# Kernel tuning notes

Measured on AMD Instinct MI355X. Metric: run time of the kernel, lower is better.

Reference implementation:

```python
import jax, jax.numpy as jnp
import numpy as np

D = 128  # h_dim == in_dim

def _gat_layer(h, d, src, dst, n_dst, W, U, V, a):
    # h: [N_src, Din], d: [E, 1], src/dst: [E]
    z = h @ W.T          # [N_src, D]
    zi = h @ U.T         # [N_src, D]
    t = d @ V.T          # [E, 1]
    Dh = W.shape[0]
    # attn_fc on concat([z_src, z_dst, t]) split into three partial dots
    e = z[src] @ a[:Dh] + z[dst] @ a[Dh:2 * Dh] + t[:, 0] * a[2 * Dh]
    e = jax.nn.leaky_relu(e)  # [E]
    # segment softmax over incoming edges of each dst node
    m = jax.ops.segment_max(e, dst, num_segments=n_dst)
    ex = jnp.exp(e - m[dst])
    s = jax.ops.segment_sum(ex, dst, num_segments=n_dst)
    alpha = ex / s[dst]  # [E]
    zn = jax.ops.segment_sum(alpha[:, None] * z[src], dst, num_segments=n_dst)
    return jax.nn.relu(zi[:n_dst] + zn)


def setup_inputs() -> dict:
    key = jax.random.key(0)
    ks = jax.random.split(key, 16)
    N0, ND0, ND1 = 100000, 40000, 20000
    E0, E1 = 640000, 320000
    sc = 1.0 / np.sqrt(D)
    inp = {
        "attr": jax.random.normal(ks[0], (N0, D), jnp.float32),
        "d0": jax.random.normal(ks[1], (E0, 1), jnp.float32),
        "d1": jax.random.normal(ks[2], (E1, 1), jnp.float32),
        "src0": jax.random.randint(ks[3], (E0,), 0, N0, jnp.int32),
        "dst0": jax.random.randint(ks[4], (E0,), 0, ND0, jnp.int32),
        "src1": jax.random.randint(ks[5], (E1,), 0, ND0, jnp.int32),
        "dst1": jax.random.randint(ks[6], (E1,), 0, ND1, jnp.int32),
        "n_dst0": ND0,
        "n_dst1": ND1,
        "W0": jax.random.normal(ks[7], (D, D), jnp.float32) * sc,
        "U0": jax.random.normal(ks[8], (D, D), jnp.float32) * sc,
        "V0": jax.random.normal(ks[9], (1, 1), jnp.float32),
        "a0": jax.random.normal(ks[10], (2 * D + 1,), jnp.float32) * sc,
        "W1": jax.random.normal(ks[11], (D, D), jnp.float32) * sc,
        "U1": jax.random.normal(ks[12], (D, D), jnp.float32) * sc,
        "V1": jax.random.normal(ks[13], (1, 1), jnp.float32),
        "a1": jax.random.normal(ks[14], (2 * D + 1,), jnp.float32) * sc,
    }
    return inp


def reference(attr, d0, d1, W0, U0, V0, a0, W1, U1, V1, a1,
              src0, dst0, src1, dst1, n_dst0, n_dst1):
    h = _gat_layer(attr, d0, src0, dst0, n_dst0, W0, U0, V0, a0)
    h = _gat_layer(h, d1, src1, dst1, n_dst1, W1, U1, V1, a1)
    return h
```

## Files before the change

kernel.cpp:

```cpp
#include <hip/hip_runtime.h>
#include <math.h>


#define D 128

typedef __bf16 bf16x8 __attribute__((ext_vector_type(8)));
typedef float f32x4 __attribute__((ext_vector_type(4)));

static __device__ __forceinline__ float lrelu(float x) {
  return x >= 0.f ? x : 0.01f * x;
}
static __device__ __forceinline__ unsigned short f2bf(float v) {
  unsigned int u = __float_as_uint(v);
  u += 0x7fffu + ((u >> 16) & 1u);
  return (unsigned short)(u >> 16);
}
static __device__ __forceinline__ float bf2f(unsigned short b) {
  return __uint_as_float((unsigned int)b << 16);
}

static __device__ __forceinline__ float4 loadV4(const float* p) {
  return *(const float4*)p;
}
static __device__ __forceinline__ float4 loadV4(const unsigned short* p) {
  ushort4 t = *(const ushort4*)p;
  return make_float4(bf2f(t.x), bf2f(t.y), bf2f(t.z), bf2f(t.w));
}
static __device__ __forceinline__ void storeV4(float* p, float4 v) {
  *(float4*)p = v;
}
static __device__ __forceinline__ void storeV4(unsigned short* p, float4 v) {
  ushort4 t;
  t.x = f2bf(v.x);
  t.y = f2bf(v.y);
  t.z = f2bf(v.z);
  t.w = f2bf(v.w);
  *(ushort4*)p = t;
}
static __device__ __forceinline__ void storeZi(float* p, float v) { *p = v; }
static __device__ __forceinline__ void storeZi(unsigned short* p, float v) {
  *p = f2bf(v);
}

static __device__ __forceinline__ int swz(int row, int colb) {
  return row * 256 + (colb ^ ((row & 7) << 4));
}

static __device__ __forceinline__ void count4(const int* __restrict__ dstC,
                                              int* __restrict__ cntC,
                                              int* __restrict__ rankC,
                                              int gid, int qC) {
  if (gid >= qC) return;
  int i0 = gid * 4;
  int4 d4 = *(const int4*)(dstC + i0);
  int4 r4;
  r4.x = atomicAdd(&cntC[d4.x], 1);
  r4.y = atomicAdd(&cntC[d4.y], 1);
  r4.z = atomicAdd(&cntC[d4.z], 1);
  r4.w = atomicAdd(&cntC[d4.w], 1);
  *(int4*)(rankC + i0) = r4;
}

__global__ __launch_bounds__(256) void cvt4_kernel(
    const float* __restrict__ s0, const float* __restrict__ s1,
    const float* __restrict__ s2, const float* __restrict__ s3,
    __bf16* __restrict__ dst) {
  int idx = blockIdx.x * 256 + threadIdx.x;
  const float* s = (idx < 16384) ? s0
                   : (idx < 32768) ? s1
                   : (idx < 49152) ? s2 : s3;
  dst[idx] = (__bf16)s[idx & 16383];
}

__global__ void zero_int_kernel(int* __restrict__ p, int n) {
  int i = blockIdx.x * 256 + threadIdx.x;
  if (i < n) p[i] = 0;
}

static __device__ __forceinline__ void stageA(const float* A, int rblk,
                                              int rlim, int t,
                                              unsigned char* ldsA) {
  const char* base = (const char*)A + (size_t)rblk * 512;
#pragma unroll
  for (int g = 0; g < 8; ++g) {
    int sb = g * 4096 + t * 16;
    float4 v = make_float4(0.f, 0.f, 0.f, 0.f);
    if (rblk + (sb >> 9) < rlim) v = *(const float4*)(base + sb);
    int db = sb >> 1;
    int row = db >> 8, colb = db & 255;
    ushort4 o;
    o.x = f2bf(v.x);
    o.y = f2bf(v.y);
    o.z = f2bf(v.z);
    o.w = f2bf(v.w);
    *(ushort4*)(&ldsA[swz(row, colb)]) = o;
  }
}
static __device__ __forceinline__ void stageA(const unsigned short* A,
                                              int rblk, int rlim, int t,
                                              unsigned char* ldsA) {
  const char* base = (const char*)A + (size_t)rblk * 256;
#pragma unroll
  for (int g = 0; g < 4; ++g) {
    int bi = g * 4096 + t * 16;
    int row = bi >> 8, colb = bi & 255;
    ushort4 lo = {0, 0, 0, 0}, hi = {0, 0, 0, 0};
    if (rblk + row < rlim) {
      lo = *(const ushort4*)(base + bi);
      hi = *(const ushort4*)(base + bi + 8);
    }
    *(ushort4*)(&ldsA[swz(row, colb)]) = lo;
    *(ushort4*)(&ldsA[swz(row, colb) + 8]) = hi;
  }
}

template <typename AT, typename ZiT>
__global__ __launch_bounds__(256, 3) void gemm_count(
    const AT* __restrict__ A, const __bf16* __restrict__ Wb,
    const __bf16* __restrict__ Ub, unsigned short* __restrict__ z,
    ZiT* __restrict__ zi, const float* __restrict__ a,
    float* __restrict__ zs, float* __restrict__ zd, int n_wb, int rows,
    int ndst, const int* __restrict__ dstC, int* __restrict__ cntC,
    int* __restrict__ rankC, int qC, int IL, int nC) {
  __shared__ unsigned char lds[49152];
  const int blk = blockIdx.x;
  const int t = threadIdx.x;

  if ((blk % IL) == 0 && (blk / IL) < nC) {
    count4(dstC, cntC, rankC, (blk / IL) * 256 + t, qC);
    return;
  }
  const int cb = min(nC, (blk + IL - 1) / IL);
  const int gb = blk - cb;

  const bool isU = (gb >= n_wb);
  const int rblk = (isU ? gb - n_wb : gb) * 64;
  const int rlim = isU ? ndst : rows;
  const __bf16* B = isU ? Ub : Wb;

#pragma unroll
  for (int g = 0; g < 8; ++g) {
    int bi = g * 4096 + t * 16;
    int row = bi >> 8, colb = bi & 255;
    bf16x8 v = *(const bf16x8*)((const char*)B + bi);
    *(bf16x8*)(&lds[swz(row, colb)]) = v;
  }
  stageA(A, rblk, rlim, t, lds + 32768);
  __syncthreads();

  const int wave = t >> 6;
  const int lane = t & 63;
  const int lm = lane & 15;
  const int lk = lane >> 4;
  const int r0 = rblk + wave * 16;
  if (r0 >= rlim) return;

  bf16x8 af[4];
#pragma unroll
  for (int kt = 0; kt < 4; ++kt) {
    int row = wave * 16 + lm;
    af[kt] = *(const bf16x8*)(&lds[32768 + swz(row, kt * 64 + lk * 16)]);
  }

  f32x4 acc[8];
#pragma unroll
  for (int tt = 0; tt < 8; ++tt) acc[tt] = (f32x4){0.f, 0.f, 0.f, 0.f};
#pragma unroll
  for (int kt = 0; kt < 4; ++kt) {
#pragma unroll
    for (int tt = 0; tt < 8; ++tt) {
      int row = tt * 16 + lm;
      bf16x8 bf = *(const bf16x8*)(&lds[swz(row, kt * 64 + lk * 16)]);
      acc[tt] =
          __builtin_amdgcn_mfma_f32_16x16x32_bf16(af[kt], bf, acc[tt], 0, 0, 0);
    }
  }

  if (!isU) {
#pragma unroll
    for (int tt = 0; tt < 8; ++tt)
#pragma unroll
      for (int rr = 0; rr < 4; ++rr)
        z[(size_t)(r0 + lk * 4 + rr) * D + tt * 16 + lm] = f2bf(acc[tt][rr]);

    float p1[4] = {0.f, 0.f, 0.f, 0.f};
    float p2[4] = {0.f, 0.f, 0.f, 0.f};
#pragma unroll
    for (int tt = 0; tt < 8; ++tt) {
      float a1 = a[tt * 16 + lm];
      float a2 = a[D + tt * 16 + lm];
#pragma unroll
      for (int rr = 0; rr < 4; ++rr) {
        p1[rr] += acc[tt][rr] * a1;
        p2[rr] += acc[tt][rr] * a2;
      }
    }
#pragma unroll
    for (int rr = 0; rr < 4; ++rr) {
#pragma unroll
      for (int o = 1; o < 16; o <<= 1) {
        p1[rr] += __shfl_xor(p1[rr], o);
        p2[rr] += __shfl_xor(p2[rr], o);
      }
      if (lm == 0) {
        zs[r0 + lk * 4 + rr] = p1[rr];
        zd[r0 + lk * 4 + rr] = p2[rr];
      }
    }
  } else {
#pragma unroll
    for (int tt = 0; tt < 8; ++tt)
#pragma unroll
      for (int rr = 0; rr < 4; ++rr)
        storeZi(&zi[(size_t)(r0 + lk * 4 + rr) * D + tt * 16 + lm],
                acc[tt][rr]);
  }
}

__global__ __launch_bounds__(256) void scan_partial(const int* __restrict__ cnt,
                                                    int* __restrict__ part,
                                                    int n) {
  __shared__ int sm[4];
  int base = blockIdx.x * 1024;
  int t = threadIdx.x;
  int s = 0;
#pragma unroll
  for (int i = 0; i < 4; ++i) {
    int idx = base + t + i * 256;
    s += (idx < n) ? cnt[idx] : 0;
  }
  for (int o = 32; o; o >>= 1) s += __shfl_xor(s, o);
  if ((t & 63) == 0) sm[t >> 6] = s;
  __syncthreads();
  if (t == 0) part[blockIdx.x] = sm[0] + sm[1] + sm[2] + sm[3];
}

__global__ __launch_bounds__(256) void scan_final(
    const int* __restrict__ cnt, const int* __restrict__ part,
    int* __restrict__ offs, int nb, int n, int total) {
  __shared__ int sm[4];
  __shared__ int sbase;
  int base = blockIdx.x * 1024;
  int t = threadIdx.x;
  if (t < 64) {
    int v = (t < nb && t < (int)blockIdx.x) ? part[t] : 0;
#pragma unroll
    for (int o = 32; o; o >>= 1) v += __shfl_xor(v, o);
    if (t == 0) sbase = v;
  }
  int idx = base + t * 4;
  int c0 = (idx + 0 < n) ? cnt[idx + 0] : 0;
  int c1 = (idx + 1 < n) ? cnt[idx + 1] : 0;
  int c2 = (idx + 2 < n) ? cnt[idx + 2] : 0;
  int c3 = (idx + 3 < n) ? cnt[idx + 3] : 0;
  int ts = c0 + c1 + c2 + c3;
  int v = ts;
#pragma unroll
  for (int o = 1; o < 64; o <<= 1) {
    int u = __shfl_up(v, o);
    if ((t & 63) >= o) v += u;
  }
  if ((t & 63) == 63) sm[t >> 6] = v;
  __syncthreads();
  int w = t >> 6;
  int waveoff = 0;
  if (w > 0) waveoff += sm[0];
  if (w > 1) waveoff += sm[1];
  if (w > 2) waveoff += sm[2];
  int run = v - ts + waveoff + sbase;
  if (idx + 0 < n) { offs[idx + 0] = run; run += c0; }
  if (idx + 1 < n) { offs[idx + 1] = run; run += c1; }
  if (idx + 2 < n) { offs[idx + 2] = run; run += c2; }
  if (idx + 3 < n) { offs[idx + 3] = run; run += c3; }
  if (blockIdx.x == 0 && t == 0) offs[n] = total;
}

__global__ void scatter_count(const int* __restrict__ src,
                              const int* __restrict__ dst,
                              const float* __restrict__ dE,
                              const float* __restrict__ zs,
                              const float* __restrict__ zd,
                              const float* __restrict__ V,
                              const float* __restrict__ a,
                              const int* __restrict__ rank,
                              const int* __restrict__ offs,
                              int2* __restrict__ csr, int E,
                              const int* __restrict__ dstC,
                              int* __restrict__ cntC, int* __restrict__ rankC,
                              int qC, int IL, int nC) {
  const int blk = blockIdx.x;
  const int t = threadIdx.x;
  if ((blk % IL) == 0 && (blk / IL) < nC) {
    count4(dstC, cntC, rankC, (blk / IL) * 256 + t, qC);
    return;
  }
  const int cb = min(nC, (blk + IL - 1) / IL);
  const int sb = blk - cb;

  int i0 = (sb * 256 + t) * 4;
  float vc = V[0] * a[2 * D];
  if (i0 + 4 <= E) {
    int4 s4 = *(const int4*)(src + i0);
    int4 d4 = *(const int4*)(dst + i0);
    float4 de = *(const float4*)(dE + i0);
    int4 r4 = *(const int4*)(rank + i0);
    float zs0 = zs[s4.x], zs1 = zs[s4.y], zs2 = zs[s4.z], zs3 = zs[s4.w];
    float zd0 = zd[d4.x], zd1 = zd[d4.y], zd2 = zd[d4.z], zd3 = zd[d4.w];
    int p0 = offs[d4.x] + r4.x;
    int p1 = offs[d4.y] + r4.y;
    int p2 = offs[d4.z] + r4.z;
    int p3 = offs[d4.w] + r4.w;
    float w0 = __expf(lrelu(zs0 + zd0 + de.x * vc));
    float w1 = __expf(lrelu(zs1 + zd1 + de.y * vc));
    float w2 = __expf(lrelu(zs2 + zd2 + de.z * vc));
    float w3 = __expf(lrelu(zs3 + zd3 + de.w * vc));
    csr[p0] = make_int2(s4.x, __float_as_int(w0));
    csr[p1] = make_int2(s4.y, __float_as_int(w1));
    csr[p2] = make_int2(s4.z, __float_as_int(w2));
    csr[p3] = make_int2(s4.w, __float_as_int(w3));
  } else {
    for (int i = i0; i < E; ++i) {
      int di = dst[i];
      int pp = offs[di] + rank[i];
      float w = __expf(lrelu(zs[src[i]] + zd[di] + dE[i] * vc));
      csr[pp] = make_int2(src[i], __float_as_int(w));
    }
  }
}

template <typename OT>
__global__ __launch_bounds__(256) void gat_perdst(
    const unsigned short* __restrict__ z, const int2* __restrict__ csr,
    const int* __restrict__ offs, const OT* __restrict__ ziin,
    OT* __restrict__ hout, int nd) {
  int n = blockIdx.x * 8 + (threadIdx.x >> 5);
  if (n >= nd) return;
  int lane = threadIdx.x & 31;
  int beg = offs[n], end = offs[n + 1];

  float s0 = 0.f, s1 = 0.f;
  float4 acc0 = make_float4(0.f, 0.f, 0.f, 0.f);
  float4 acc1 = make_float4(0.f, 0.f, 0.f, 0.f);
  const unsigned short* zp = z + lane * 4;
  int j = beg;
  for (; j + 8 <= end; j += 8) {
    int2 pr[8];
#pragma unroll
    for (int u = 0; u < 8; ++u) pr[u] = csr[j + u];
    float4 zv[8];
#pragma unroll
    for (int u = 0; u < 8; ++u) zv[u] = loadV4(zp + (size_t)pr[u].x * D);
#pragma unroll
    for (int u = 0; u < 8; u += 2) {
      float wa = __int_as_float(pr[u].y);
      float wb = __int_as_float(pr[u + 1].y);
      s0 += wa;
      acc0.x += wa * zv[u].x;
      acc0.y += wa * zv[u].y;
      acc0.z += wa * zv[u].z;
      acc0.w += wa * zv[u].w;
      s1 += wb;
      acc1.x += wb * zv[u + 1].x;
      acc1.y += wb * zv[u + 1].y;
      acc1.z += wb * zv[u + 1].z;
      acc1.w += wb * zv[u + 1].w;
    }
  }
  for (; j < end; ++j) {
    int2 pr = csr[j];
    float w = __int_as_float(pr.y);
    float4 zv = loadV4(zp + (size_t)pr.x * D);
    s0 += w;
    acc0.x += w * zv.x;
    acc0.y += w * zv.y;
    acc0.z += w * zv.z;
    acc0.w += w * zv.w;
  }
  float s = s0 + s1;
  float inv = (s > 0.f) ? 1.f / s : 0.f;
  float4 acc = make_float4(acc0.x + acc1.x, acc0.y + acc1.y, acc0.z + acc1.z,
                           acc0.w + acc1.w);
  float4 ziv = loadV4(ziin + (size_t)n * D + lane * 4);
  float4 o4;
  o4.x = fmaxf(ziv.x + acc.x * inv, 0.f);
  o4.y = fmaxf(ziv.y + acc.y * inv, 0.f);
  o4.z = fmaxf(ziv.z + acc.z * inv, 0.f);
  o4.w = fmaxf(ziv.w + acc.w * inv, 0.f);
  storeV4(hout + (size_t)n * D + lane * 4, o4);
}

extern "C" void kernel_launch(void* const* d_in, const int* in_sizes, int n_in,
                              void* d_out, int out_size, void* d_ws,
                              size_t ws_size, hipStream_t stream) {
  const float* attr = (const float*)d_in[0];
  const float* d0 = (const float*)d_in[1];
  const float* d1 = (const float*)d_in[2];
  const int* src0 = (const int*)d_in[3];
  const int* dst0 = (const int*)d_in[4];
  const int* src1 = (const int*)d_in[5];
  const int* dst1 = (const int*)d_in[6];
  const float* W0 = (const float*)d_in[9];
  const float* U0 = (const float*)d_in[10];
  const float* V0 = (const float*)d_in[11];
  const float* a0 = (const float*)d_in[12];
  const float* W1 = (const float*)d_in[13];
  const float* U1 = (const float*)d_in[14];
  const float* V1 = (const float*)d_in[15];
  const float* a1 = (const float*)d_in[16];

  const int N0 = in_sizes[0] / D;
  const int E0 = in_sizes[1];
  const int E1 = in_sizes[2];
  const int ND0 = 40000;
  const int ND1 = 20000;

  char* p = (char*)d_ws;
  auto alloc = [&](size_t bytes) {
    char* q = p;
    p += (bytes + 255) & ~(size_t)255;
    return q;
  };
  unsigned short* z = (unsigned short*)alloc((size_t)N0 * D * 2);
  int2* csr = (int2*)alloc((size_t)E0 * 8);
  unsigned short* h1b = (unsigned short*)alloc((size_t)ND0 * D * 2);
  int* rank0 = (int*)alloc((size_t)E0 * 4);
  int* rank1 = (int*)alloc((size_t)E1 * 4);
  float* zs = (float*)alloc((size_t)N0 * 4);
  float* zd = (float*)alloc((size_t)N0 * 4);
  int* offs0 = (int*)alloc((size_t)(ND0 + 1) * 4);
  int* offs1 = (int*)alloc((size_t)(ND1 + 1) * 4);
  int* cnt01 = (int*)alloc((size_t)(ND0 + ND1) * 4);
  int* part = (int*)alloc((size_t)64 * 4);
  __bf16* wb = (__bf16*)alloc((size_t)4 * D * D * 2);
  int* cnt0 = cnt01;
  int* cnt1 = cnt01 + ND0;
  (void)n_in;
  (void)out_size;
  (void)ws_size;

  float* out = (float*)d_out;

  cvt4_kernel<<<256, 256, 0, stream>>>(W0, U0, W1, U1, wb);
  zero_int_kernel<<<(ND0 + ND1 + 255) / 256, 256, 0, stream>>>(cnt01,
                                                               ND0 + ND1);
  const __bf16* W0b = wb;
  const __bf16* U0b = wb + 16384;
  const __bf16* W1b = wb + 32768;
  const __bf16* U1b = wb + 49152;

  {
    int q0 = E0 / 4;
    int nC = (q0 + 255) / 256;
    int n_wb = (N0 + 63) / 64;
    int n_ub = (ND0 + 63) / 64;
    int total = n_wb + n_ub + nC;
    int IL = total / nC;
    gemm_count<float, unsigned short><<<total, 256, 0, stream>>>(
        attr, W0b, U0b, z, (unsigned short*)d_out, a0, zs, zd, n_wb, N0, ND0,
        dst0, cnt0, rank0, q0, IL, nC);
  }
  {
    int nb = (ND0 + 1023) / 1024;
    scan_partial<<<nb, 256, 0, stream>>>(cnt0, part, ND0);
    scan_final<<<nb, 256, 0, stream>>>(cnt0, part, offs0, nb, ND0, E0);
  }
  {
    int q1 = E1 / 4;
    int nC = (q1 + 255) / 256;
    int nS = (E0 / 4 + 255) / 256;
    int total = nS + nC;
    int IL = total / nC;
    scatter_count<<<total, 256, 0, stream>>>(src0, dst0, d0, zs, zd, V0, a0,
                                             rank0, offs0, csr, E0, dst1,
                                             cnt1, rank1, q1, IL, nC);
  }
  gat_perdst<unsigned short><<<(ND0 + 7) / 8, 256, 0, stream>>>(
      z, csr, offs0, (const unsigned short*)d_out, h1b, ND0);

  {
    int n_wb = (ND0 + 63) / 64, n_ub = (ND1 + 63) / 64;
    gemm_count<unsigned short, float><<<n_wb + n_ub, 256, 0, stream>>>(
        h1b, W1b, U1b, z, out, a1, zs, zd, n_wb, ND0, ND1, nullptr, nullptr,
        nullptr, 0, 1, 0);
  }
  {
    int nb = (ND1 + 1023) / 1024;
    scan_partial<<<nb, 256, 0, stream>>>(cnt1, part, ND1);
    scan_final<<<nb, 256, 0, stream>>>(cnt1, part, offs1, nb, ND1, E1);
  }
  scatter_count<<<(E1 / 4 + 255) / 256, 256, 0, stream>>>(
      src1, dst1, d1, zs, zd, V1, a1, rank1, offs1, csr, E1, nullptr, nullptr,
      nullptr, 0, 1, 0);
  gat_perdst<float><<<(ND1 + 7) / 8, 256, 0, stream>>>(z, csr, offs1, out, out,
                                                       ND1);
}
```

Before: 156.4 us.

## Move layer-1 degree counting into aggregation kernel and widen per-lane features

Merges the weight-conversion and counter-zeroing kernels into one launch. Moves the layer-1 in-degree count out of the layer-0 scatter and interleaves it with the layer-0 per-destination aggregation blocks. Each destination node now uses 16 lanes holding 8 features each, instead of 32 lanes holding 4, with an unroll of 4 edges. The aim is to cut launches, balance work across kernels, and raise memory-level parallelism per lane. The cost is more registers per thread and fewer outstanding edges per unroll.

```diff
diff --git a/kernel.cpp b/kernel.cpp
--- a/kernel.cpp
+++ b/kernel.cpp
@@ -6,6 +6,10 @@
 
 typedef __bf16 bf16x8 __attribute__((ext_vector_type(8)));
 typedef float f32x4 __attribute__((ext_vector_type(4)));
+
+struct F8 {
+  float4 lo, hi;
+};
 
 static __device__ __forceinline__ float lrelu(float x) {
   return x >= 0.f ? x : 0.01f * x;
@@ -19,23 +23,30 @@
   return __uint_as_float((unsigned int)b << 16);
 }
 
-static __device__ __forceinline__ float4 loadV4(const float* p) {
-  return *(const float4*)p;
-}
-static __device__ __forceinline__ float4 loadV4(const unsigned short* p) {
-  ushort4 t = *(const ushort4*)p;
-  return make_float4(bf2f(t.x), bf2f(t.y), bf2f(t.z), bf2f(t.w));
-}
-static __device__ __forceinline__ void storeV4(float* p, float4 v) {
-  *(float4*)p = v;
-}
-static __device__ __forceinline__ void storeV4(unsigned short* p, float4 v) {
-  ushort4 t;
-  t.x = f2bf(v.x);
-  t.y = f2bf(v.y);
-  t.z = f2bf(v.z);
-  t.w = f2bf(v.w);
-  *(ushort4*)p = t;
+static __device__ __forceinline__ F8 loadV8(const float* p) {
+  F8 r;
+  r.lo = *(const float4*)p;
+  r.hi = *(const float4*)(p + 4);
+  return r;
+}
+static __device__ __forceinline__ F8 loadV8(const unsigned short* p) {
+  ushort4 a = *(const ushort4*)p;
+  ushort4 b = *(const ushort4*)(p + 4);
+  F8 r;
+  r.lo = make_float4(bf2f(a.x), bf2f(a.y), bf2f(a.z), bf2f(a.w));
+  r.hi = make_float4(bf2f(b.x), bf2f(b.y), bf2f(b.z), bf2f(b.w));
+  return r;
+}
+static __device__ __forceinline__ void storeV8(float* p, F8 v) {
+  *(float4*)p = v.lo;
+  *(float4*)(p + 4) = v.hi;
+}
+static __device__ __forceinline__ void storeV8(unsigned short* p, F8 v) {
+  ushort4 a, b;
+  a.x = f2bf(v.lo.x); a.y = f2bf(v.lo.y); a.z = f2bf(v.lo.z); a.w = f2bf(v.lo.w);
+  b.x = f2bf(v.hi.x); b.y = f2bf(v.hi.y); b.z = f2bf(v.hi.z); b.w = f2bf(v.hi.w);
+  *(ushort4*)p = a;
+  *(ushort4*)(p + 4) = b;
 }
 static __device__ __forceinline__ void storeZi(float* p, float v) { *p = v; }
 static __device__ __forceinline__ void storeZi(unsigned short* p, float v) {
@@ -61,20 +72,19 @@
   *(int4*)(rankC + i0) = r4;
 }
 
-__global__ __launch_bounds__(256) void cvt4_kernel(
+__global__ __launch_bounds__(256) void cvt4_zero_kernel(
     const float* __restrict__ s0, const float* __restrict__ s1,
     const float* __restrict__ s2, const float* __restrict__ s3,
-    __bf16* __restrict__ dst) {
+    __bf16* __restrict__ dst, int* __restrict__ cnt, int nz) {
   int idx = blockIdx.x * 256 + threadIdx.x;
-  const float* s = (idx < 16384) ? s0
-                   : (idx < 32768) ? s1
-                   : (idx < 49152) ? s2 : s3;
-  dst[idx] = (__bf16)s[idx & 16383];
-}
-
-__global__ void zero_int_kernel(int* __restrict__ p, int n) {
-  int i = blockIdx.x * 256 + threadIdx.x;
-  if (i < n) p[i] = 0;
+  if (idx < 65536) {
+    const float* s = (idx < 16384) ? s0
+                     : (idx < 32768) ? s1
+                     : (idx < 49152) ? s2 : s3;
+    dst[idx] = (__bf16)s[idx & 16383];
+  } else if (idx - 65536 < nz) {
+    cnt[idx - 65536] = 0;
+  }
 }
 
 static __device__ __forceinline__ void stageA(const float* A, int rblk,
@@ -275,29 +285,17 @@
   if (blockIdx.x == 0 && t == 0) offs[n] = total;
 }
 
-__global__ void scatter_count(const int* __restrict__ src,
-                              const int* __restrict__ dst,
-                              const float* __restrict__ dE,
-                              const float* __restrict__ zs,
-                              const float* __restrict__ zd,
-                              const float* __restrict__ V,
-                              const float* __restrict__ a,
-                              const int* __restrict__ rank,
-                              const int* __restrict__ offs,
-                              int2* __restrict__ csr, int E,
-                              const int* __restrict__ dstC,
-                              int* __restrict__ cntC, int* __restrict__ rankC,
-                              int qC, int IL, int nC) {
-  const int blk = blockIdx.x;
-  const int t = threadIdx.x;
-  if ((blk % IL) == 0 && (blk / IL) < nC) {
-    count4(dstC, cntC, rankC, (blk / IL) * 256 + t, qC);
-    return;
-  }
-  const int cb = min(nC, (blk + IL - 1) / IL);
-  const int sb = blk - cb;
-
-  int i0 = (sb * 256 + t) * 4;
+__global__ void scatter_w_kernel(const int* __restrict__ src,
+                                 const int* __restrict__ dst,
+                                 const float* __restrict__ dE,
+                                 const float* __restrict__ zs,
+                                 const float* __restrict__ zd,
+                                 const float* __restrict__ V,
+                                 const float* __restrict__ a,
+                                 const int* __restrict__ rank,
+                                 const int* __restrict__ offs,
+                                 int2* __restrict__ csr, int E) {
+  int i0 = (blockIdx.x * 256 + threadIdx.x) * 4;
   float vc = V[0] * a[2 * D];
   if (i0 + 4 <= E) {
     int4 s4 = *(const int4*)(src + i0);
@@ -329,64 +327,94 @@
 }
 
 template <typename OT>
-__global__ __launch_bounds__(256) void gat_perdst(
+__global__ __launch_bounds__(256) void gat_perdst_count(
     const unsigned short* __restrict__ z, const int2* __restrict__ csr,
     const int* __restrict__ offs, const OT* __restrict__ ziin,
-    OT* __restrict__ hout, int nd) {
-  int n = blockIdx.x * 8 + (threadIdx.x >> 5);
+    OT* __restrict__ hout, int nd, const int* __restrict__ dstC,
+    int* __restrict__ cntC, int* __restrict__ rankC, int qC, int IL, int nC) {
+  const int blk = blockIdx.x;
+  const int t = threadIdx.x;
+  if ((blk % IL) == 0 && (blk / IL) < nC) {
+    count4(dstC, cntC, rankC, (blk / IL) * 256 + t, qC);
+    return;
+  }
+  const int cb = min(nC, (blk + IL - 1) / IL);
+  const int ab = blk - cb;
+
+  int n = ab * 16 + (t >> 4);
   if (n >= nd) return;
-  int lane = threadIdx.x & 31;
+  int lane = t & 15;
   int beg = offs[n], end = offs[n + 1];
 
   float s0 = 0.f, s1 = 0.f;
-  float4 acc0 = make_float4(0.f, 0.f, 0.f, 0.f);
-  float4 acc1 = make_float4(0.f, 0.f, 0.f, 0.f);
-  const unsigned short* zp = z + lane * 4;
+  F8 acc0, acc1;
+  acc0.lo = acc0.hi = make_float4(0.f, 0.f, 0.f, 0.f);
+  acc1.lo = acc1.hi = make_float4(0.f, 0.f, 0.f, 0.f);
+  const unsigned short* zp = z + lane * 8;
   int j = beg;
-  for (; j + 8 <= end; j += 8) {
-    int2 pr[8];
-#pragma unroll
-    for (int u = 0; u < 8; ++u) pr[u] = csr[j + u];
-    float4 zv[8];
-#pragma unroll
-    for (int u = 0; u < 8; ++u) zv[u] = loadV4(zp + (size_t)pr[u].x * D);
-#pragma unroll
-    for (int u = 0; u < 8; u += 2) {
+  for (; j + 4 <= end; j += 4) {
+    int2 pr[4];
+#pragma unroll
+    for (int u = 0; u < 4; ++u) pr[u] = csr[j + u];
+    F8 zv[4];
+#pragma unroll
+    for (int u = 0; u < 4; ++u) zv[u] = loadV8(zp + (size_t)pr[u].x * D);
+#pragma unroll
+    for (int u = 0; u < 4; u += 2) {
       float wa = __int_as_float(pr[u].y);
       float wb = __int_as_float(pr[u + 1].y);
       s0 += wa;
-      acc0.x += wa * zv[u].x;
-      acc0.y += wa * zv[u].y;
-      acc0.z += wa * zv[u].z;
-      acc0.w += wa * zv[u].w;
+      acc0.lo.x += wa * zv[u].lo.x;
+      acc0.lo.y += wa * zv[u].lo.y;
+      acc0.lo.z += wa * zv[u].lo.z;
+      acc0.lo.w += wa * zv[u].lo.w;
+      acc0.hi.x += wa * zv[u].hi.x;
+      acc0.hi.y += wa * zv[u].hi.y;
+      acc0.hi.z += wa * zv[u].hi.z;
+      acc0.hi.w += wa * zv[u].hi.w;
       s1 += wb;
-      acc1.x += wb * zv[u + 1].x;
-      acc1.y += wb * zv[u + 1].y;
-      acc1.z += wb * zv[u + 1].z;
-      acc1.w += wb * zv[u + 1].w;
+      acc1.lo.x += wb * zv[u + 1].lo.x;
+      acc1.lo.y += wb * zv[u + 1].lo.y;
+      acc1.lo.z += wb * zv[u + 1].lo.z;
+      acc1.lo.w += wb * zv[u + 1].lo.w;
+      acc1.hi.x += wb * zv[u + 1].hi.x;
+      acc1.hi.y += wb * zv[u + 1].hi.y;
+      acc1.hi.z += wb * zv[u + 1].hi.z;
+      acc1.hi.w += wb * zv[u + 1].hi.w;
     }
   }
   for (; j < end; ++j) {
     int2 pr = csr[j];
     float w = __int_as_float(pr.y);
-    float4 zv = loadV4(zp + (size_t)pr.x * D);
+    F8 zv = loadV8(zp + (size_t)pr.x * D);
     s0 += w;
-    acc0.x += w * zv.x;
-    acc0.y += w * zv.y;
-    acc0.z += w * zv.z;
-    acc0.w += w * zv.w;
+    acc0.lo.x += w * zv.lo.x;
+    acc0.lo.y += w * zv.lo.y;
+    acc0.lo.z += w * zv.lo.z;
+    acc0.lo.w += w * zv.lo.w;
+    acc0.hi.x += w * zv.hi.x;
+    acc0.hi.y += w * zv.hi.y;
+    acc0.hi.z += w * zv.hi.z;
+    acc0.hi.w += w * zv.hi.w;
   }
   float s = s0 + s1;
   float inv = (s > 0.f) ? 1.f / s : 0.f;
-  float4 acc = make_float4(acc0.x + acc1.x, acc0.y + acc1.y, acc0.z + acc1.z,
-                           acc0.w + acc1.w);
-  float4 ziv = loadV4(ziin + (size_t)n * D + lane * 4);
-  float4 o4;
-  o4.x = fmaxf(ziv.x + acc.x * inv, 0.f);
-  o4.y = fmaxf(ziv.y + acc.y * inv, 0.f);
-  o4.z = fmaxf(ziv.z + acc.z * inv, 0.f);
-  o4.w = fmaxf(ziv.w + acc.w * inv, 0.f);
-  storeV4(hout + (size_t)n * D + lane * 4, o4);
+  F8 acc;
+  acc.lo = make_float4(acc0.lo.x + acc1.lo.x, acc0.lo.y + acc1.lo.y,
+                       acc0.lo.z + acc1.lo.z, acc0.lo.w + acc1.lo.w);
+  acc.hi = make_float4(acc0.hi.x + acc1.hi.x, acc0.hi.y + acc1.hi.y,
+                       acc0.hi.z + acc1.hi.z, acc0.hi.w + acc1.hi.w);
+  F8 ziv = loadV8(ziin + (size_t)n * D + lane * 8);
+  F8 o;
+  o.lo.x = fmaxf(ziv.lo.x + acc.lo.x * inv, 0.f);
+  o.lo.y = fmaxf(ziv.lo.y + acc.lo.y * inv, 0.f);
+  o.lo.z = fmaxf(ziv.lo.z + acc.lo.z * inv, 0.f);
+  o.lo.w = fmaxf(ziv.lo.w + acc.lo.w * inv, 0.f);
+  o.hi.x = fmaxf(ziv.hi.x + acc.hi.x * inv, 0.f);
+  o.hi.y = fmaxf(ziv.hi.y + acc.hi.y * inv, 0.f);
+  o.hi.z = fmaxf(ziv.hi.z + acc.hi.z * inv, 0.f);
+  o.hi.w = fmaxf(ziv.hi.w + acc.hi.w * inv, 0.f);
+  storeV8(hout + (size_t)n * D + lane * 8, o);
 }
 
 extern "C" void kernel_launch(void* const* d_in, const int* in_sizes, int n_in,
@@ -440,9 +468,11 @@
 
   float* out = (float*)d_out;
 
-  cvt4_kernel<<<256, 256, 0, stream>>>(W0, U0, W1, U1, wb);
-  zero_int_kernel<<<(ND0 + ND1 + 255) / 256, 256, 0, stream>>>(cnt01,
-                                                               ND0 + ND1);
+  {
+    int tot = 65536 + ND0 + ND1;
+    cvt4_zero_kernel<<<(tot + 255) / 256, 256, 0, stream>>>(
+        W0, U0, W1, U1, wb, cnt01, ND0 + ND1);
+  }
   const __bf16* W0b = wb;
   const __bf16* U0b = wb + 16384;
   const __bf16* W1b = wb + 32768;
@@ -464,19 +494,18 @@
     scan_partial<<<nb, 256, 0, stream>>>(cnt0, part, ND0);
     scan_final<<<nb, 256, 0, stream>>>(cnt0, part, offs0, nb, ND0, E0);
   }
+  scatter_w_kernel<<<(E0 / 4 + 255) / 256, 256, 0, stream>>>(
+      src0, dst0, d0, zs, zd, V0, a0, rank0, offs0, csr, E0);
   {
     int q1 = E1 / 4;
     int nC = (q1 + 255) / 256;
-    int nS = (E0 / 4 + 255) / 256;
-    int total = nS + nC;
+    int nA = (ND0 + 15) / 16;
+    int total = nA + nC;
     int IL = total / nC;
-    scatter_count<<<total, 256, 0, stream>>>(src0, dst0, d0, zs, zd, V0, a0,
-                                             rank0, offs0, csr, E0, dst1,
-                                             cnt1, rank1, q1, IL, nC);
-  }
-  gat_perdst<unsigned short><<<(ND0 + 7) / 8, 256, 0, stream>>>(
-      z, csr, offs0, (const unsigned short*)d_out, h1b, ND0);
-
+    gat_perdst_count<unsigned short><<<total, 256, 0, stream>>>(
+        z, csr, offs0, (const unsigned short*)d_out, h1b, ND0, dst1, cnt1,
+        rank1, q1, IL, nC);
+  }
   {
     int n_wb = (ND0 + 63) / 64, n_ub = (ND1 + 63) / 64;
     gemm_count<unsigned short, float><<<n_wb + n_ub, 256, 0, stream>>>(
@@ -488,9 +517,8 @@
     scan_partial<<<nb, 256, 0, stream>>>(cnt1, part, ND1);
     scan_final<<<nb, 256, 0, stream>>>(cnt1, part, offs1, nb, ND1, E1);
   }
-  scatter_count<<<(E1 / 4 + 255) / 256, 256, 0, stream>>>(
-      src1, dst1, d1, zs, zd, V1, a1, rank1, offs1, csr, E1, nullptr, nullptr,
-      nullptr, 0, 1, 0);
-  gat_perdst<float><<<(ND1 + 7) / 8, 256, 0, stream>>>(z, csr, offs1, out, out,
-                                                       ND1);
-}
+  scatter_w_kernel<<<(E1 / 4 + 255) / 256, 256, 0, stream>>>(
+      src1, dst1, d1, zs, zd, V1, a1, rank1, offs1, csr, E1);
+  gat_perdst_count<float><<<((ND1 + 15) / 16), 256, 0, stream>>>(
+      z, csr, offs1, out, out, ND1, nullptr, nullptr, nullptr, 0, 1, 0);
+}
```

Result: no change. 158.5 us (+1.3%).
